# Performance work log

Measured on AMD Instinct MI355X. Metric: run time of the kernel, lower is better.

## Reference

```python
import jax, jax.numpy as jnp
import numpy as np

B, S, E = 4, 1024, 1024
H, DH = 16, 64
P = 64  # prompt length
MASKED_BIAS = -10000.0


def setup_inputs() -> dict:
    key = jax.random.key(0)
    ks = jax.random.split(key, 9)
    return {
        "hidden_states": jax.random.normal(ks[0], (B, S, E), jnp.float32),
        "promptKey": jax.random.normal(ks[1], (B, H, P, DH), jnp.float32),
        "promptValue": jax.random.normal(ks[2], (B, H, P, DH), jnp.float32),
        "textualKey": jax.random.normal(ks[3], (B, H, S, DH), jnp.float32),
        "textualValue": jax.random.normal(ks[4], (B, H, S, DH), jnp.float32),
        "promptMask": jnp.ones((B, 1, S, P), jnp.bool_),
        "c_attn_w": jax.random.normal(ks[5], (E, 3 * E), jnp.float32) * 0.02,
        "c_attn_b": jnp.zeros((3 * E,), jnp.float32),
        "c_proj_w": jax.random.normal(ks[6], (E, E), jnp.float32) * 0.02,
        "c_proj_b": jnp.zeros((E,), jnp.float32),
    }


def _split_heads(t):
    # [B, S, E] -> [B, H, S, DH]
    b, s, _ = t.shape
    return t.reshape(b, s, H, DH).transpose(0, 2, 1, 3)


def reference(hidden_states, promptKey, promptValue, textualKey, textualValue,
              promptMask, c_attn_w, c_attn_b, c_proj_w, c_proj_b):
    qkv = hidden_states @ c_attn_w + c_attn_b          # [B,S,3E]
    q, k, v = jnp.split(qkv, 3, axis=-1)
    q, k, v = _split_heads(q), _split_heads(k), _split_heads(v)  # [B,H,S,DH]

    # scores against prompt KV, textual KV, and elementwise self term
    promptW = jnp.einsum("bhsd,bhpd->bhsp", q, promptKey)       # [B,H,S,P]
    textW = jnp.einsum("bhsd,bhtd->bhst", q, textualKey)        # [B,H,S,S]
    selfW = jnp.sum(q * k, axis=-1, keepdims=True)              # [B,H,S,1]
    attn_weights = jnp.concatenate((promptW, textW, selfW), axis=-1)
    attn_weights = attn_weights / jnp.sqrt(jnp.float32(DH))

    # non-residual causal mask: bias[qlen-qlen:qlen, 1:klen+1] -> strictly lower tri
    causal = jnp.tri(S, S, -1, dtype=bool)                      # [S,S]
    self_mask = jnp.ones((S, 1), dtype=bool)
    causal_self = jnp.concatenate((causal, self_mask), axis=-1)[None, None]  # [1,1,S,S+1]
    full_mask = jnp.concatenate(
        (promptMask, jnp.broadcast_to(causal_self, (B, 1, S, S + 1))), axis=-1)
    attn_weights = jnp.where(full_mask, attn_weights, MASKED_BIAS)
    attn_weights = jax.nn.softmax(attn_weights, axis=-1)

    wSelf = attn_weights[..., -1:]                              # [B,H,S,1]
    wRest = attn_weights[..., :-1]                              # [B,H,S,P+S]
    valuePast = jnp.concatenate((promptValue, textualValue), axis=-2)  # [B,H,P+S,DH]
    attn_output = jnp.einsum("bhsk,bhkd->bhsd", wRest, valuePast) + wSelf * v

    # merge heads and output projection
    attn_output = attn_output.transpose(0, 2, 1, 3).reshape(B, S, E)
    return attn_output @ c_proj_w + c_proj_b
```

## Files before the change

kernel.cpp:

```cpp
#include <hip/hip_runtime.h>
#include <hip/hip_bf16.h>
#include <stdint.h>

#define H_ 16
#define DH_ 64
#define S_ 1024
#define B_ 4
#define E_ 1024
#define P_ 64
#define BH_ (B_ * H_)
#define KV_ (P_ + S_)
#define NT_ 17
#define TILE_ELEMS 4096

typedef __attribute__((ext_vector_type(8))) short short8;
typedef __attribute__((ext_vector_type(4))) float floatx4;

#define MFMA_BF16(a, b, c) __builtin_amdgcn_mfma_f32_16x16x32_bf16((a), (b), (c), 0, 0, 0)

__device__ __forceinline__ float bf2f(unsigned short u) {
    union { float f; uint32_t i; } x;
    x.i = ((uint32_t)u) << 16;
    return x.f;
}
__device__ __forceinline__ unsigned short f2bf(float f) {
    uint32_t i = __float_as_uint(f);
    uint32_t r = (i + 0x7fffu + ((i >> 16) & 1u)) >> 16;
    return (unsigned short)r;
}

__device__ __forceinline__ void gl_lds16(const void* g, void* l) {
    __builtin_amdgcn_global_load_lds(
        (const __attribute__((address_space(1))) uint32_t*)g,
        (__attribute__((address_space(3))) uint32_t*)l, 16, 0, 0);
}

#define BARRIER() asm volatile("s_barrier" ::: "memory")
#define WAIT_VM(n) asm volatile("s_waitcnt vmcnt(" #n ")" ::: "memory")

__global__ void prep(const float* __restrict__ hidden, const float* __restrict__ cw,
                     const float* __restrict__ pw, const float* __restrict__ pK,
                     const float* __restrict__ tK, const float* __restrict__ pV,
                     const float* __restrict__ tV, unsigned short* __restrict__ Ah,
                     unsigned short* __restrict__ Wt1, unsigned short* __restrict__ Wt2,
                     unsigned short* __restrict__ Kp, unsigned short* __restrict__ Vp) {
    __shared__ float t[32][33];
    int bid = blockIdx.x, tid = threadIdx.x;
    if (bid < 4096) {
        int i = bid * 256 + tid;
        float4 v = ((const float4*)hidden)[i];
        ushort4 o;
        o.x = f2bf(v.x); o.y = f2bf(v.y); o.z = f2bf(v.z); o.w = f2bf(v.w);
        ((ushort4*)Ah)[i] = o;
    } else if (bid < 8192) {
        const float* in; unsigned short* out; int R, C, bxx, byy;
        if (bid < 7168) { int i = bid - 4096; in = cw; out = Wt1; R = 1024; C = 3072; bxx = i % 96; byy = i / 96; }
        else            { int i = bid - 7168; in = pw; out = Wt2; R = 1024; C = 1024; bxx = i % 32; byy = i / 32; }
        int tx = tid & 31, ty = tid >> 5;
        int c0 = bxx * 32, r0 = byy * 32;
#pragma unroll
        for (int i = 0; i < 4; ++i)
            t[ty + i * 8][tx] = in[(size_t)(r0 + ty + i * 8) * C + c0 + tx];
        __syncthreads();
#pragma unroll
        for (int i = 0; i < 4; ++i)
            out[(size_t)(c0 + ty + i * 8) * R + r0 + tx] = f2bf(t[tx][ty + i * 8]);
    } else {
        int gid0 = (bid - 8192) * 256 + tid;
        int half = gid0 / (BH_ * 8704);
        int gid = gid0 % (BH_ * 8704);
        int bh = gid / 8704, rem = gid % 8704;
        int tt = rem / 512, r2 = rem % 512;
        int f = r2 >> 6, lane = r2 & 63;
        int nt = f >> 1, h = f & 1, quad = lane >> 4, cl = lane & 15;
        unsigned short o[8];
        if (half == 0) {
            int key = tt * 64 + nt * 16 + cl;
            int dh = h * 32 + quad * 8;
            const float* src = (key < P_)
                ? pK + ((size_t)bh * P_ + key) * DH_ + dh
                : tK + ((size_t)bh * S_ + (key - P_)) * DH_ + dh;
#pragma unroll
            for (int u = 0; u < 8; ++u) o[u] = f2bf(src[u]);
            *(int4*)&Kp[(size_t)gid * 8] = *(int4*)o;
        } else {
            int dhn = nt * 16 + cl;
            int kbase = tt * 64 + h * 32 + quad * 8;
            const float* src = (kbase < P_)
                ? pV + ((size_t)bh * P_ + kbase) * DH_ + dhn
                : tV + ((size_t)bh * S_ + (kbase - P_)) * DH_ + dhn;
#pragma unroll
            for (int u = 0; u < 8; ++u) o[u] = f2bf(src[(size_t)u * DH_]);
            *(int4*)&Vp[(size_t)gid * 8] = *(int4*)o;
        }
    }
}

template <int MODE, int TM, int TN, int BK>
__global__ __launch_bounds__(256) void gemm_bt(
    const unsigned short* __restrict__ A, const unsigned short* __restrict__ Bt,
    const float* __restrict__ bias, float* __restrict__ Cout,
    unsigned short* __restrict__ Qo, unsigned short* __restrict__ Ko,
    unsigned short* __restrict__ Vo, int M, int N, int K) {
    constexpr int MI = TM / 32, NI = TN / 32;
    constexpr int NA = TM * BK / 2048;
    constexpr int NB = TN * BK / 2048;
    static_assert(NA + NB == 4, "vmcnt constant assumes 4 loads/tile");
    __shared__ __align__(16) unsigned short lA[2][TM * BK];
    __shared__ __align__(16) unsigned short lB[2][TN * BK];
    int tid = threadIdx.x;
    int wave = tid >> 6, lane = tid & 63, quad = lane >> 4, cl = lane & 15;
    int m0 = blockIdx.y * TM, n0 = blockIdx.x * TN;
    int wm = (wave >> 1) * (TM / 2), wn = (wave & 1) * (TN / 2);
    floatx4 acc[MI][NI];
#pragma unroll
    for (int mi = 0; mi < MI; ++mi)
#pragma unroll
        for (int ni = 0; ni < NI; ++ni) acc[mi][ni] = (floatx4){0.f, 0.f, 0.f, 0.f};

    auto issue = [&](int k0, int buf) {
#pragma unroll
        for (int li = 0; li < NA; ++li) {
            int o = (li * 256 + tid) * 16;
            int hh = o / (TM * 64), rr = (o % (TM * 64)) >> 6, c8 = (o >> 4) & 3;
            gl_lds16(A + (size_t)(m0 + rr) * K + k0 + hh * 32 + c8 * 8,
                     (char*)lA[buf] + o);
        }
#pragma unroll
        for (int li = 0; li < NB; ++li) {
            int o = (li * 256 + tid) * 16;
            int hh = o / (TN * 64), rr = (o % (TN * 64)) >> 6, c8 = (o >> 4) & 3;
            gl_lds16(Bt + (size_t)(n0 + rr) * K + k0 + hh * 32 + c8 * 8,
                     (char*)lB[buf] + o);
        }
    };
    auto compute = [&](int buf) {
#pragma unroll
        for (int kk = 0; kk < BK / 32; ++kk) {
            short8 af[MI], bfr[NI];
#pragma unroll
            for (int mi = 0; mi < MI; ++mi)
                af[mi] = *(const short8*)&lA[buf][kk * TM * 32 + (wm + mi * 16 + cl) * 32 + quad * 8];
#pragma unroll
            for (int ni = 0; ni < NI; ++ni)
                bfr[ni] = *(const short8*)&lB[buf][kk * TN * 32 + (wn + ni * 16 + cl) * 32 + quad * 8];
#pragma unroll
            for (int mi = 0; mi < MI; ++mi)
#pragma unroll
                for (int ni = 0; ni < NI; ++ni)
                    acc[mi][ni] = MFMA_BF16(af[mi], bfr[ni], acc[mi][ni]);
        }
    };

    int nT = K / BK;
    issue(0, 0);
    for (int t = 0; t < nT; ++t) {
        int buf = t & 1;
        if (t + 1 < nT) {
            issue((t + 1) * BK, buf ^ 1);
            WAIT_VM(4);
        } else {
            WAIT_VM(0);
        }
        BARRIER();
        compute(buf);
        BARRIER();
    }

#pragma unroll
    for (int ni = 0; ni < NI; ++ni) {
        int ncol = n0 + wn + ni * 16 + cl;
        float bv = bias[ncol];
#pragma unroll
        for (int mi = 0; mi < MI; ++mi) {
#pragma unroll
            for (int r = 0; r < 4; ++r) {
                int mrow = m0 + wm + mi * 16 + quad * 4 + r;
                float v = acc[mi][ni][r] + bv;
                if (MODE == 0) {
                    Cout[(size_t)mrow * N + ncol] = v;
                } else {
                    int which = ncol >> 10, e = ncol & 1023;
                    int hh = e >> 6, dh = e & 63;
                    int b = mrow >> 10, s = mrow & 1023;
                    size_t idx = ((size_t)(b * H_ + hh) * S_ + s) * DH_ + dh;
                    unsigned short* dst = (which == 0) ? Qo : ((which == 1) ? Ko : Vo);
                    dst[idx] = f2bf(v);
                }
            }
        }
    }
}

__global__ __launch_bounds__(256) void attn_k(
    const unsigned short* __restrict__ Q, const unsigned short* __restrict__ Kc,
    const unsigned short* __restrict__ Vc, const unsigned short* __restrict__ Kp,
    const unsigned short* __restrict__ Vp, unsigned short* __restrict__ Aout) {
    __shared__ __align__(16) unsigned short lK[TILE_ELEMS];
    __shared__ __align__(16) unsigned short lV[TILE_ELEMS];
    __shared__ __align__(16) unsigned short lP[4][16 * 72];
    int tid = threadIdx.x, wave = tid >> 6, lane = tid & 63;
    int quad = lane >> 4, cl = lane & 15;
    int l = blockIdx.x;
    int p = l >> 6, bh = l & 63;
    int b = bh >> 4, h = bh & 15;
    const unsigned short* Qb = Q + (size_t)bh * S_ * DH_;
    const unsigned short* Kb = Kc + (size_t)bh * S_ * DH_;
    const unsigned short* Vb = Vc + (size_t)bh * S_ * DH_;
    const unsigned short* Kpb = Kp + (size_t)bh * NT_ * TILE_ELEMS;
    const unsigned short* Vpb = Vp + (size_t)bh * NT_ * TILE_ELEMS;
    unsigned short* lp = lP[wave];
    int so = wave * 1024 + lane * 16;

    int x1 = p, x2 = 15 - p;
    int qb1 = x1 * 64 + wave * 16, qb2 = x2 * 64 + wave * 16;

    short8 a0_1 = *(const short8*)(Qb + (size_t)(qb1 + cl) * DH_ + quad * 8);
    short8 a1_1 = *(const short8*)(Qb + (size_t)(qb1 + cl) * DH_ + quad * 8 + 32);
    short8 a0_2 = *(const short8*)(Qb + (size_t)(qb2 + cl) * DH_ + quad * 8);
    short8 a1_2 = *(const short8*)(Qb + (size_t)(qb2 + cl) * DH_ + quad * 8 + 32);

    float lsum1[4] = {0.f, 0.f, 0.f, 0.f}, lsum2[4] = {0.f, 0.f, 0.f, 0.f};
    floatx4 O1[4], O2[4];
#pragma unroll
    for (int nt = 0; nt < 4; ++nt) {
        O1[nt] = (floatx4){0.f, 0.f, 0.f, 0.f};
        O2[nt] = (floatx4){0.f, 0.f, 0.f, 0.f};
    }

    int rl = wave * 16 + quad * 4;

    auto do_tile = [&](short8 a0, short8 a1, floatx4* O, float* lsum, bool diag) {
        floatx4 s[4];
#pragma unroll
        for (int nt = 0; nt < 4; ++nt) {
            s[nt] = (floatx4){0.f, 0.f, 0.f, 0.f};
            short8 k0 = *(const short8*)&lK[(nt * 2 + 0) * 512 + lane * 8];
            short8 k1 = *(const short8*)&lK[(nt * 2 + 1) * 512 + lane * 8];
            s[nt] = MFMA_BF16(a0, k0, s[nt]);
            s[nt] = MFMA_BF16(a1, k1, s[nt]);
        }
#pragma unroll
        for (int nt = 0; nt < 4; ++nt) {
            int col = nt * 16 + cl;
#pragma unroll
            for (int r = 0; r < 4; ++r) {
                float v = s[nt][r] * 0.125f;
                if (diag && col >= rl + r) v = -10000.0f;
                float pb = __expf(v);
                lsum[r] += pb;
                lp[(quad * 4 + r) * 72 + col] = f2bf(pb);
            }
        }
        asm volatile("s_waitcnt lgkmcnt(0)" ::: "memory");
        short8 p0 = *(const short8*)&lp[cl * 72 + quad * 8];
        short8 p1 = *(const short8*)&lp[cl * 72 + quad * 8 + 32];
#pragma unroll
        for (int nt = 0; nt < 4; ++nt) {
            short8 v0 = *(const short8*)&lV[(nt * 2 + 0) * 512 + lane * 8];
            short8 v1 = *(const short8*)&lV[(nt * 2 + 1) * 512 + lane * 8];
            O[nt] = MFMA_BF16(p0, v0, O[nt]);
            O[nt] = MFMA_BF16(p1, v1, O[nt]);
        }
    };

    int T1 = x1 + 2, Tu = x2 + 2;
    for (int t = 0; t < Tu; ++t) {
        __syncthreads();
        {
            const char* gK = (const char*)(Kpb + (size_t)t * TILE_ELEMS);
            const char* gV = (const char*)(Vpb + (size_t)t * TILE_ELEMS);
            gl_lds16(gK + so, (char*)lK + so);
            gl_lds16(gK + 4096 + so, (char*)lK + 4096 + so);
            gl_lds16(gV + so, (char*)lV + so);
            gl_lds16(gV + 4096 + so, (char*)lV + 4096 + so);
        }
        __syncthreads();

        do_tile(a0_2, a1_2, O2, lsum2, t == Tu - 1);
        if (t < T1) do_tile(a0_1, a1_1, O1, lsum1, t == T1 - 1);
    }

#pragma unroll
    for (int seg = 0; seg < 2; ++seg) {
        int qb = seg ? qb2 : qb1;
        float* lsum = seg ? lsum2 : lsum1;
        floatx4* O = seg ? O2 : O1;
#pragma unroll
        for (int r = 0; r < 4; ++r) {
            float rs = lsum[r];
            rs += __shfl_xor(rs, 1, 16);
            rs += __shfl_xor(rs, 2, 16);
            rs += __shfl_xor(rs, 4, 16);
            rs += __shfl_xor(rs, 8, 16);
            int row = qb + quad * 4 + r;
            const unsigned short* qp = Qb + (size_t)row * DH_ + cl * 4;
            const unsigned short* kp = Kb + (size_t)row * DH_ + cl * 4;
            float d = 0.f;
#pragma unroll
            for (int u = 0; u < 4; ++u) d += bf2f(qp[u]) * bf2f(kp[u]);
            d += __shfl_xor(d, 1, 16);
            d += __shfl_xor(d, 2, 16);
            d += __shfl_xor(d, 4, 16);
            d += __shfl_xor(d, 8, 16);
            float ps = __expf(d * 0.125f);
            float linv = 1.0f / (rs + ps);
#pragma unroll
            for (int nt = 0; nt < 4; ++nt) {
                float vv = bf2f(Vb[(size_t)row * DH_ + nt * 16 + cl]);
                float o = (O[nt][r] + ps * vv) * linv;
                Aout[((size_t)b * S_ + row) * E_ + h * DH_ + nt * 16 + cl] = f2bf(o);
            }
        }
    }
}

extern "C" void kernel_launch(void* const* d_in, const int* in_sizes, int n_in,
                              void* d_out, int out_size, void* d_ws, size_t ws_size,
                              hipStream_t stream) {
    const float* hidden = (const float*)d_in[0];
    const float* pK = (const float*)d_in[1];
    const float* pV = (const float*)d_in[2];
    const float* tK = (const float*)d_in[3];
    const float* tV = (const float*)d_in[4];
    const float* cw = (const float*)d_in[6];
    const float* cb = (const float*)d_in[7];
    const float* pw = (const float*)d_in[8];
    const float* pb = (const float*)d_in[9];
    float* out = (float*)d_out;

    unsigned short* ws = (unsigned short*)d_ws;
    unsigned short* Wt1 = ws;
    unsigned short* Wt2 = Wt1 + (size_t)3072 * 1024;
    unsigned short* Ah  = Wt2 + (size_t)1024 * 1024;
    unsigned short* Qw  = Ah + (size_t)4096 * 1024;
    unsigned short* Kw  = Qw + (size_t)BH_ * S_ * DH_;
    unsigned short* Vw  = Kw + (size_t)BH_ * S_ * DH_;
    unsigned short* Kp  = Vw + (size_t)BH_ * S_ * DH_;
    unsigned short* Vp  = Kp + (size_t)BH_ * NT_ * TILE_ELEMS;
    unsigned short* At  = Ah;

    prep<<<12544, 256, 0, stream>>>(hidden, cw, pw, pK, tK, pV, tV,
                                    Ah, Wt1, Wt2, Kp, Vp);
    gemm_bt<1, 128, 128, 32><<<dim3(3072 / 128, 4096 / 128), 256, 0, stream>>>(
        Ah, Wt1, cb, nullptr, Qw, Kw, Vw, 4096, 3072, 1024);
    attn_k<<<512, 256, 0, stream>>>(Qw, Kw, Vw, Kp, Vp, At);
    gemm_bt<0, 64, 64, 64><<<dim3(1024 / 64, 4096 / 128 * 2), 256, 0, stream>>>(
        At, Wt2, pb, out, nullptr, nullptr, nullptr, 4096, 1024, 1024);
}
```

Baseline: 199.9 us.

## Add 256x256 8-wave QKV GEMM, double-buffer attention KV tiles, retile out-proj

Replaces the QKV projection with a new 256x256-tile, 512-thread GEMM kernel. It uses XOR-swizzled LDS, a double-buffered global-to-LDS pipeline split into half-K stages, setprio around the MFMA bursts, and a grid swizzle for L2 locality. The attention kernel now double-buffers its K/V tiles so the next tile's loads overlap compute, instead of syncing around each load. The output projection switches to 128x128x32 tiles. The larger tiles and double buffers raise register and LDS pressure and cut the QKV grid to 192 blocks, which may leave some compute units idle.

```diff
diff --git a/kernel.cpp b/kernel.cpp
--- a/kernel.cpp
+++ b/kernel.cpp
@@ -37,6 +37,7 @@
 
 #define BARRIER() asm volatile("s_barrier" ::: "memory")
 #define WAIT_VM(n) asm volatile("s_waitcnt vmcnt(" #n ")" ::: "memory")
+#define LGKM0() asm volatile("s_waitcnt lgkmcnt(0)" ::: "memory")
 
 __global__ void prep(const float* __restrict__ hidden, const float* __restrict__ cw,
                      const float* __restrict__ pw, const float* __restrict__ pK,
@@ -192,12 +193,140 @@
     }
 }
 
+__global__ __launch_bounds__(512, 2) void gemm8_qkv(
+    const unsigned short* __restrict__ A, const unsigned short* __restrict__ Bt,
+    const float* __restrict__ bias, unsigned short* __restrict__ Qo,
+    unsigned short* __restrict__ Ko, unsigned short* __restrict__ Vo,
+    int M, int N, int K, int nbx) {
+    __shared__ __align__(16) unsigned short sm[4][16384];
+    int tid = threadIdx.x;
+    int wave = tid >> 6, lane = tid & 63, quad = lane >> 4, cl = lane & 15;
+    int cpx = gridDim.x >> 3;
+    int swzb = ((int)blockIdx.x & 7) * cpx + ((int)blockIdx.x >> 3);
+    int m0 = (swzb / nbx) * 256, n0 = (swzb % nbx) * 256;
+    int wm = (wave >> 2) * 128, wn = (wave & 3) * 64;
+    int cq = quad ^ ((cl >> 1) & 3);
+
+    auto stage = [&](const unsigned short* __restrict__ G, int row0, int k0,
+                     unsigned short* l) {
+#pragma unroll
+        for (int li = 0; li < 4; ++li) {
+            int idx = li * 512 + tid;
+            int kh = idx >> 10;
+            int r = (idx >> 2) & 255;
+            int c = (idx & 3) ^ ((r >> 1) & 3);
+            gl_lds16(G + (size_t)(row0 + r) * K + k0 + kh * 32 + c * 8,
+                     (char*)l + idx * 16);
+        }
+    };
+
+    floatx4 acc[8][4];
+#pragma unroll
+    for (int mi = 0; mi < 8; ++mi)
+#pragma unroll
+        for (int ni = 0; ni < 4; ++ni) acc[mi][ni] = (floatx4){0.f, 0.f, 0.f, 0.f};
+
+    int nT = K / 64;
+    stage(A, m0, 0, sm[0]);
+    stage(Bt, n0, 0, sm[1]);
+    WAIT_VM(0);
+    BARRIER();
+
+    for (int j = 0; j < nT; ++j) {
+        const unsigned short* sa = sm[(j & 1) * 2];
+        const unsigned short* sb = sm[(j & 1) * 2 + 1];
+        unsigned short* na = sm[((j & 1) ^ 1) * 2];
+        unsigned short* nb = sm[((j & 1) ^ 1) * 2 + 1];
+        short8 af[4], bf0[4], bf1[4];
+
+#pragma unroll
+        for (int ni = 0; ni < 4; ++ni)
+            bf0[ni] = *(const short8*)(sb + (wn + ni * 16 + cl) * 32 + cq * 8);
+#pragma unroll
+        for (int mi = 0; mi < 4; ++mi)
+            af[mi] = *(const short8*)(sa + (wm + mi * 16 + cl) * 32 + cq * 8);
+        if (j + 1 < nT) stage(A, m0, (j + 1) * 64, na);
+        BARRIER(); LGKM0();
+        __builtin_amdgcn_s_setprio(1);
+#pragma unroll
+        for (int mi = 0; mi < 4; ++mi)
+#pragma unroll
+            for (int ni = 0; ni < 4; ++ni)
+                acc[mi][ni] = MFMA_BF16(af[mi], bf0[ni], acc[mi][ni]);
+        __builtin_amdgcn_s_setprio(0);
+        BARRIER();
+
+#pragma unroll
+        for (int ni = 0; ni < 4; ++ni)
+            bf1[ni] = *(const short8*)(sb + 8192 + (wn + ni * 16 + cl) * 32 + cq * 8);
+#pragma unroll
+        for (int mi = 0; mi < 4; ++mi)
+            af[mi] = *(const short8*)(sa + 8192 + (wm + mi * 16 + cl) * 32 + cq * 8);
+        if (j + 1 < nT) stage(Bt, n0, (j + 1) * 64, nb);
+        BARRIER(); LGKM0();
+        __builtin_amdgcn_s_setprio(1);
+#pragma unroll
+        for (int mi = 0; mi < 4; ++mi)
+#pragma unroll
+            for (int ni = 0; ni < 4; ++ni)
+                acc[mi][ni] = MFMA_BF16(af[mi], bf1[ni], acc[mi][ni]);
+        __builtin_amdgcn_s_setprio(0);
+        BARRIER();
+
+#pragma unroll
+        for (int mi = 0; mi < 4; ++mi)
+            af[mi] = *(const short8*)(sa + (wm + 64 + mi * 16 + cl) * 32 + cq * 8);
+        BARRIER(); LGKM0();
+        __builtin_amdgcn_s_setprio(1);
+#pragma unroll
+        for (int mi = 0; mi < 4; ++mi)
+#pragma unroll
+            for (int ni = 0; ni < 4; ++ni)
+                acc[4 + mi][ni] = MFMA_BF16(af[mi], bf0[ni], acc[4 + mi][ni]);
+        __builtin_amdgcn_s_setprio(0);
+        BARRIER();
+
+#pragma unroll
+        for (int mi = 0; mi < 4; ++mi)
+            af[mi] = *(const short8*)(sa + 8192 + (wm + 64 + mi * 16 + cl) * 32 + cq * 8);
+        BARRIER(); LGKM0();
+        __builtin_amdgcn_s_setprio(1);
+#pragma unroll
+        for (int mi = 0; mi < 4; ++mi)
+#pragma unroll
+            for (int ni = 0; ni < 4; ++ni)
+                acc[4 + mi][ni] = MFMA_BF16(af[mi], bf1[ni], acc[4 + mi][ni]);
+        __builtin_amdgcn_s_setprio(0);
+        WAIT_VM(0);
+        BARRIER();
+    }
+
+#pragma unroll
+    for (int ni = 0; ni < 4; ++ni) {
+        int ncol = n0 + wn + ni * 16 + cl;
+        float bv = bias[ncol];
+        int which = ncol >> 10, e = ncol & 1023;
+        int hh = e >> 6, dh = e & 63;
+        unsigned short* dst = (which == 0) ? Qo : ((which == 1) ? Ko : Vo);
+#pragma unroll
+        for (int mi = 0; mi < 8; ++mi) {
+#pragma unroll
+            for (int r = 0; r < 4; ++r) {
+                int mrow = m0 + wm + mi * 16 + quad * 4 + r;
+                int b = mrow >> 10, s = mrow & 1023;
+                dst[((size_t)(b * H_ + hh) * S_ + s) * DH_ + dh] =
+                    f2bf(acc[mi][ni][r] + bv);
+            }
+        }
+    }
+}
+
 __global__ __launch_bounds__(256) void attn_k(
     const unsigned short* __restrict__ Q, const unsigned short* __restrict__ Kc,
     const unsigned short* __restrict__ Vc, const unsigned short* __restrict__ Kp,
     const unsigned short* __restrict__ Vp, unsigned short* __restrict__ Aout) {
-    __shared__ __align__(16) unsigned short lK[TILE_ELEMS];
-    __shared__ __align__(16) unsigned short lV[TILE_ELEMS];
+    __shared__ __align__(16) unsigned short lK[2][TILE_ELEMS];
+    __shared__ __align__(16) unsigned short lV[2][TILE_ELEMS];
     __shared__ __align__(16) unsigned short lP[4][16 * 72];
     int tid = threadIdx.x, wave = tid >> 6, lane = tid & 63;
     int quad = lane >> 4, cl = lane & 15;
@@ -230,13 +359,23 @@
 
     int rl = wave * 16 + quad * 4;
 
-    auto do_tile = [&](short8 a0, short8 a1, floatx4* O, float* lsum, bool diag) {
+    auto issue_tile = [&](int t, int bi) {
+        const char* gK = (const char*)(Kpb + (size_t)t * TILE_ELEMS);
+        const char* gV = (const char*)(Vpb + (size_t)t * TILE_ELEMS);
+        gl_lds16(gK + so, (char*)lK[bi] + so);
+        gl_lds16(gK + 4096 + so, (char*)lK[bi] + 4096 + so);
+        gl_lds16(gV + so, (char*)lV[bi] + so);
+        gl_lds16(gV + 4096 + so, (char*)lV[bi] + 4096 + so);
+    };
+
+    auto do_tile = [&](const unsigned short* Kt, const unsigned short* Vt,
+                       short8 a0, short8 a1, floatx4* O, float* lsum, bool diag) {
         floatx4 s[4];
 #pragma unroll
         for (int nt = 0; nt < 4; ++nt) {
             s[nt] = (floatx4){0.f, 0.f, 0.f, 0.f};
-            short8 k0 = *(const short8*)&lK[(nt * 2 + 0) * 512 + lane * 8];
-            short8 k1 = *(const short8*)&lK[(nt * 2 + 1) * 512 + lane * 8];
+            short8 k0 = *(const short8*)&Kt[(nt * 2 + 0) * 512 + lane * 8];
+            short8 k1 = *(const short8*)&Kt[(nt * 2 + 1) * 512 + lane * 8];
             s[nt] = MFMA_BF16(a0, k0, s[nt]);
             s[nt] = MFMA_BF16(a1, k1, s[nt]);
         }
@@ -257,28 +396,28 @@
         short8 p1 = *(const short8*)&lp[cl * 72 + quad * 8 + 32];
 #pragma unroll
         for (int nt = 0; nt < 4; ++nt) {
-            short8 v0 = *(const short8*)&lV[(nt * 2 + 0) * 512 + lane * 8];
-            short8 v1 = *(const short8*)&lV[(nt * 2 + 1) * 512 + lane * 8];
+            short8 v0 = *(const short8*)&Vt[(nt * 2 + 0) * 512 + lane * 8];
+            short8 v1 = *(const short8*)&Vt[(nt * 2 + 1) * 512 + lane * 8];
             O[nt] = MFMA_BF16(p0, v0, O[nt]);
             O[nt] = MFMA_BF16(p1, v1, O[nt]);
         }
     };
 
     int T1 = x1 + 2, Tu = x2 + 2;
+    issue_tile(0, 0);
     for (int t = 0; t < Tu; ++t) {
-        __syncthreads();
-        {
-            const char* gK = (const char*)(Kpb + (size_t)t * TILE_ELEMS);
-            const char* gV = (const char*)(Vpb + (size_t)t * TILE_ELEMS);
-            gl_lds16(gK + so, (char*)lK + so);
-            gl_lds16(gK + 4096 + so, (char*)lK + 4096 + so);
-            gl_lds16(gV + so, (char*)lV + so);
-            gl_lds16(gV + 4096 + so, (char*)lV + 4096 + so);
-        }
-        __syncthreads();
-
-        do_tile(a0_2, a1_2, O2, lsum2, t == Tu - 1);
-        if (t < T1) do_tile(a0_1, a1_1, O1, lsum1, t == T1 - 1);
+        int bi = t & 1;
+        if (t + 1 < Tu) {
+            issue_tile(t + 1, bi ^ 1);
+            WAIT_VM(4);
+        } else {
+            WAIT_VM(0);
+        }
+        BARRIER();
+
+        do_tile(lK[bi], lV[bi], a0_2, a1_2, O2, lsum2, t == Tu - 1);
+        if (t < T1) do_tile(lK[bi], lV[bi], a0_1, a1_1, O1, lsum1, t == T1 - 1);
+        BARRIER();
     }
 
 #pragma unroll
@@ -342,9 +481,8 @@
 
     prep<<<12544, 256, 0, stream>>>(hidden, cw, pw, pK, tK, pV, tV,
                                     Ah, Wt1, Wt2, Kp, Vp);
-    gemm_bt<1, 128, 128, 32><<<dim3(3072 / 128, 4096 / 128), 256, 0, stream>>>(
-        Ah, Wt1, cb, nullptr, Qw, Kw, Vw, 4096, 3072, 1024);
+    gemm8_qkv<<<192, 512, 0, stream>>>(Ah, Wt1, cb, Qw, Kw, Vw, 4096, 3072, 1024, 12);
     attn_k<<<512, 256, 0, stream>>>(Qw, Kw, Vw, Kp, Vp, At);
-    gemm_bt<0, 64, 64, 64><<<dim3(1024 / 64, 4096 / 128 * 2), 256, 0, stream>>>(
+    gemm_bt<0, 128, 128, 32><<<dim3(1024 / 128, 4096 / 128), 256, 0, stream>>>(
         At, Wt2, pb, out, nullptr, nullptr, nullptr, 4096, 1024, 1024);
 }
```

After: 209.7 us. 4.9% more time.
